# Kernel tuning notes

Measured on AMD Instinct MI355X. Metric: run time of the kernel, lower is better.

Reference implementation:

```python
import jax, jax.numpy as jnp
import numpy as np

N = 100000      # nodes
E = 1600000     # edges (avg degree 16)
D_IN, D_H, D_OUT = 128, 128, 64
EPS = 1e-5      # BatchNorm eps


def setup_inputs() -> dict:
    key = jax.random.key(0)
    ks = jax.random.split(key, 16)
    def w(k, i, o):
        return jax.random.normal(k, (i, o), jnp.float32) / np.float32(np.sqrt(i))
    inp = {
        "x": jax.random.normal(ks[0], (N, D_IN), jnp.float32),
        "edge_index": jax.random.randint(ks[1], (2, E), 0, N, dtype=jnp.int32),
        # layer 0 (SAGEConv: lin_l on aggregated neighbors w/ bias, lin_r on root w/o bias)
        "Wl0": w(ks[2], D_IN, D_H), "bl0": jax.random.normal(ks[3], (D_H,), jnp.float32) * 0.01,
        "Wr0": w(ks[4], D_IN, D_H),
        "g0": jnp.ones((D_H,), jnp.float32), "b0": jnp.zeros((D_H,), jnp.float32),
        "m0": jax.random.normal(ks[5], (D_H,), jnp.float32) * 0.1, "v0": jnp.ones((D_H,), jnp.float32),
        # layer 1
        "Wl1": w(ks[6], D_H, D_H), "bl1": jax.random.normal(ks[7], (D_H,), jnp.float32) * 0.01,
        "Wr1": w(ks[8], D_H, D_H),
        "g1": jnp.ones((D_H,), jnp.float32), "b1": jnp.zeros((D_H,), jnp.float32),
        "m1": jax.random.normal(ks[9], (D_H,), jnp.float32) * 0.1, "v1": jnp.ones((D_H,), jnp.float32),
        # layer 2 (output)
        "Wl2": w(ks[10], D_H, D_OUT), "bl2": jax.random.normal(ks[11], (D_OUT,), jnp.float32) * 0.01,
        "Wr2": w(ks[12], D_H, D_OUT),
    }
    return inp


def _sage_conv(x, src, dst, Wl, bl, Wr):
    # mean aggregation of neighbor (source) features at destination nodes
    deg = jax.ops.segment_sum(jnp.ones((src.shape[0],), x.dtype), dst, num_segments=N)
    agg = jax.ops.segment_sum(x[src], dst, num_segments=N)  # [N, d] irregular scatter-add
    agg = agg / jnp.maximum(deg, 1.0)[:, None]
    return agg @ Wl + bl + x @ Wr


def _bn(h, g, b, m, v):
    # BatchNorm1d in eval mode (running stats)
    return g * (h - m) * jax.lax.rsqrt(v + EPS) + b


def reference(x, edge_index,
              Wl0, bl0, Wr0, g0, b0, m0, v0,
              Wl1, bl1, Wr1, g1, b1, m1, v1,
              Wl2, bl2, Wr2):
    src, dst = edge_index[0], edge_index[1]
    h = jax.nn.relu(_bn(_sage_conv(x, src, dst, Wl0, bl0, Wr0), g0, b0, m0, v0))
    h = jax.nn.relu(_bn(_sage_conv(h, src, dst, Wl1, bl1, Wr1), g1, b1, m1, v1))
    h = _sage_conv(h, src, dst, Wl2, bl2, Wr2)
    return jax.nn.log_softmax(h, axis=-1)
```

## Files before the change

kernel.cpp:

```cpp
#include <hip/hip_runtime.h>

constexpr float EPS = 1e-5f;

#define NPB_LOG 9
#define NPB 512

typedef __attribute__((ext_vector_type(8))) __bf16 bf16x8;
typedef __attribute__((ext_vector_type(4))) float f32x4;
typedef __attribute__((ext_vector_type(2))) float f32x2;

__device__ __forceinline__ float blo(unsigned u) { return __uint_as_float(u << 16); }
__device__ __forceinline__ float bhi(unsigned u) { return __uint_as_float(u & 0xffff0000u); }
__device__ __forceinline__ unsigned bf1(float f) {
    unsigned u = __float_as_uint(f);
    return (u + 0x7fffu + ((u >> 16) & 1u)) >> 16;
}
__device__ __forceinline__ unsigned pack2(float a, float b) { return bf1(a) | (bf1(b) << 16); }

__device__ __forceinline__ f32x2 fp8lo(unsigned w) {
    return __builtin_amdgcn_cvt_pk_f32_fp8(w, false);
}
__device__ __forceinline__ f32x2 fp8hi(unsigned w) {
    return __builtin_amdgcn_cvt_pk_f32_fp8(w, true);
}


__global__ void bucket_hist_kernel(const int* __restrict__ dst, int* __restrict__ bcnt,
                                   int E, int B) {
    __shared__ int h[256];
    int t = threadIdx.x;
    h[t] = 0;
    __syncthreads();
    for (int e = blockIdx.x * blockDim.x + t; e < E; e += gridDim.x * blockDim.x)
        atomicAdd(&h[dst[e] >> NPB_LOG], 1);
    __syncthreads();
    if (t < B && h[t]) atomicAdd(&bcnt[t], h[t]);
}

__global__ void bucket_scan_kernel(const int* __restrict__ bcnt, int* __restrict__ bstart,
                                   int* __restrict__ cursorB, int B, int E) {
    __shared__ int tmp[256];
    int t = threadIdx.x;
    int v = (t < B) ? bcnt[t] : 0;
    tmp[t] = v;
    __syncthreads();
    for (int off = 1; off < 256; off <<= 1) {
        int x = tmp[t];
        if (t >= off) x += tmp[t - off];
        __syncthreads();
        tmp[t] = x;
        __syncthreads();
    }
    if (t < B) {
        int ex = tmp[t] - v;
        bstart[t] = ex;
        cursorB[t] = ex;
    }
    if (t == 0) bstart[B] = E;
}

__global__ __launch_bounds__(256) void partition_kernel(
    const int* __restrict__ src, const int* __restrict__ dst,
    int* __restrict__ cursorB, unsigned* __restrict__ ebuf, int E, int B) {
    __shared__ int hist[256];
    __shared__ int base[256];
    int t = threadIdx.x;
    hist[t] = 0;
    __syncthreads();
    int e0 = blockIdx.x * 4096;
    int e1 = min(e0 + 4096, E);
    for (int e = e0 + t; e < e1; e += 256)
        atomicAdd(&hist[dst[e] >> NPB_LOG], 1);
    __syncthreads();
    int h = hist[t];
    if (t < B && h) base[t] = atomicAdd(&cursorB[t], h);
    __syncthreads();
    hist[t] = 0;
    __syncthreads();
    for (int e = e0 + t; e < e1; e += 256) {
        int d = dst[e];
        int b = d >> NPB_LOG;
        int off = atomicAdd(&hist[b], 1);
        ebuf[base[b] + off] = ((unsigned)src[e] << NPB_LOG) | (unsigned)(d & (NPB - 1));
    }
}

__global__ __launch_bounds__(256) void build_csr_kernel(
    const unsigned* __restrict__ ebuf, const int* __restrict__ bstart,
    int* __restrict__ rowptr, float* __restrict__ degInv, int* __restrict__ csr,
    int N, int B) {
    __shared__ int cnt[NPB];
    __shared__ int cur[NPB];
    __shared__ int ps[256];
    int b = blockIdx.x;
    int t = threadIdx.x;
    int nbase = b << NPB_LOG;
    int nn = min(NPB, N - nbase);
    cnt[t] = 0;
    cnt[t + 256] = 0;
    __syncthreads();
    int ebeg = bstart[b], eend = bstart[b + 1];
    for (int e = ebeg + t; e < eend; e += 256)
        atomicAdd(&cnt[ebuf[e] & (NPB - 1)], 1);
    __syncthreads();
    int c0 = cnt[2 * t], c1 = cnt[2 * t + 1];
    int pair = c0 + c1;
    ps[t] = pair;
    __syncthreads();
    for (int off = 1; off < 256; off <<= 1) {
        int x = ps[t];
        if (t >= off) x += ps[t - off];
        __syncthreads();
        ps[t] = x;
        __syncthreads();
    }
    int exPair = ps[t] - pair;
    int g0 = ebeg + exPair;
    int g1 = g0 + c0;
    cur[2 * t] = g0;
    cur[2 * t + 1] = g1;
    if (2 * t < nn) {
        rowptr[nbase + 2 * t] = g0;
        degInv[nbase + 2 * t] = 1.0f / (float)max(c0, 1);
    }
    if (2 * t + 1 < nn) {
        rowptr[nbase + 2 * t + 1] = g1;
        degInv[nbase + 2 * t + 1] = 1.0f / (float)max(c1, 1);
    }
    if (b == B - 1 && t == 0) rowptr[N] = eend;
    __syncthreads();
    for (int e = ebeg + t; e < eend; e += 256) {
        unsigned p = ebuf[e];
        int pos = atomicAdd(&cur[p & (NPB - 1)], 1);
        csr[pos] = (int)(p >> NPB_LOG);
    }
}

__global__ void cvt_bf16_kernel(const float* __restrict__ in, unsigned short* __restrict__ out,
                                int n4) {
    int i = blockIdx.x * blockDim.x + threadIdx.x;
    if (i < n4) {
        float4 v = reinterpret_cast<const float4*>(in)[i];
        uint2 o;
        o.x = pack2(v.x, v.y);
        o.y = pack2(v.z, v.w);
        reinterpret_cast<uint2*>(out)[i] = o;
    }
}

__global__ void swizzleWcat_kernel(const float* __restrict__ Wl, const float* __restrict__ Wr,
                                   unsigned short* __restrict__ out, int K, int CL, int CR) {
    int C = CL + CR;
    int CT = C >> 4;
    int total = (K >> 5) * CT * 64;
    int id = blockIdx.x * blockDim.x + threadIdx.x;
    if (id >= total) return;
    int lane = id & 63;
    int ctkt = id >> 6;
    int ct = ctkt % CT;
    int kt = ctkt / CT;
    int col = ct * 16 + (lane & 15);
    int k0 = kt * 32 + (lane >> 4) * 8;
#pragma unroll
    for (int i = 0; i < 8; ++i) {
        int k = k0 + i;
        float w = (col < CL) ? Wl[(size_t)k * CL + col] : Wr[(size_t)k * CR + (col - CL)];
        out[(size_t)id * 8 + i] = (unsigned short)bf1(w);
    }
}

__global__ void bnprep_kernel(const float* __restrict__ g, const float* __restrict__ b,
                              const float* __restrict__ m, const float* __restrict__ v,
                              float* __restrict__ bnA, float* __restrict__ bnB, int D) {
    int c = blockIdx.x * blockDim.x + threadIdx.x;
    if (c < D) {
        float A = g[c] * rsqrtf(v[c] + EPS);
        bnA[c] = A;
        bnB[c] = b[c] - m[c] * A;
    }
}

template <int CHALF>
__global__ __launch_bounds__(256) void gemmT_kernel(
    const unsigned short* __restrict__ A, const unsigned short* __restrict__ Wsw,
    const float* __restrict__ bl,
    unsigned char* __restrict__ tL, unsigned short* __restrict__ tR, int n) {
    constexpr int CT = CHALF / 16;
    int tid = threadIdx.x;
    int lane = tid & 63;
    int wave = tid >> 6;
    int wr = wave >> 1, wc = wave & 1;
    int row0 = blockIdx.x * 64 + wr * 32;
    int rlo = lane & 15, kq = lane >> 4;

    f32x4 acc[2][CT];
#pragma unroll
    for (int nt = 0; nt < 2; ++nt)
#pragma unroll
        for (int c = 0; c < CT; ++c)
#pragma unroll
            for (int k = 0; k < 4; ++k) acc[nt][c][k] = 0.f;

    int r0 = row0 + rlo;
    int r1 = row0 + 16 + rlo;

    for (int kt = 0; kt < 4; ++kt) {
        int kb = kt * 32 + kq * 8;
        bf16x8 a0, a1;
#pragma unroll
        for (int i = 0; i < 8; ++i) { a0[i] = (__bf16)0.f; a1[i] = (__bf16)0.f; }
        if (r0 < n) a0 = *reinterpret_cast<const bf16x8*>(A + (size_t)r0 * 128 + kb);
        if (r1 < n) a1 = *reinterpret_cast<const bf16x8*>(A + (size_t)r1 * 128 + kb);
#pragma unroll
        for (int c = 0; c < CT; ++c) {
            int ct_g = wc * CT + c;
            bf16x8 w = *reinterpret_cast<const bf16x8*>(Wsw + ((size_t)(kt * 2 * CT + ct_g) * 64 + lane) * 8);
            acc[0][c] = __builtin_amdgcn_mfma_f32_16x16x32_bf16(w, a0, acc[0][c], 0, 0, 0);
            acc[1][c] = __builtin_amdgcn_mfma_f32_16x16x32_bf16(w, a1, acc[1][c], 0, 0, 0);
        }
    }

#pragma unroll
    for (int nt = 0; nt < 2; ++nt) {
        int r = row0 + nt * 16 + rlo;
        if (r >= n) continue;
#pragma unroll
        for (int c = 0; c < CT; ++c) {
            int colbase = c * 16 + kq * 4;
            if (wc == 0) {
                unsigned w = __builtin_amdgcn_cvt_pk_fp8_f32(acc[nt][c][0], acc[nt][c][1], 0, false);
                w = __builtin_amdgcn_cvt_pk_fp8_f32(acc[nt][c][2], acc[nt][c][3], w, true);
                *reinterpret_cast<unsigned*>(tL + (size_t)r * CHALF + colbase) = w;
            } else {
                float4 bv = *reinterpret_cast<const float4*>(bl + colbase);
                uint2 o;
                o.x = pack2(acc[nt][c][0] + bv.x, acc[nt][c][1] + bv.y);
                o.y = pack2(acc[nt][c][2] + bv.z, acc[nt][c][3] + bv.w);
                *reinterpret_cast<uint2*>(tR + (size_t)r * CHALF + colbase) = o;
            }
        }
    }
}

__global__ void aggbn_kernel(const unsigned char* __restrict__ tL,
                             const unsigned short* __restrict__ tR,
                             const float* __restrict__ bnA, const float* __restrict__ bnB,
                             const int* __restrict__ rowptr, const int* __restrict__ csr,
                             const float* __restrict__ degInv,
                             unsigned short* __restrict__ h, int n) {
    int idx = blockIdx.x * blockDim.x + threadIdx.x;
    int v = idx >> 4;
    int t = idx & 15;
    if (v >= n) return;
    int beg = rowptr[v], end = rowptr[v + 1];
    const uint2* T2 = reinterpret_cast<const uint2*>(tL);
    float s0 = 0.f, s1 = 0.f, s2 = 0.f, s3 = 0.f, s4 = 0.f, s5 = 0.f, s6 = 0.f, s7 = 0.f;
    int e = beg;
    for (; e + 4 <= end; e += 4) {
        uint2 w0 = T2[(size_t)csr[e + 0] * 16 + t];
        uint2 w1 = T2[(size_t)csr[e + 1] * 16 + t];
        uint2 w2 = T2[(size_t)csr[e + 2] * 16 + t];
        uint2 w3 = T2[(size_t)csr[e + 3] * 16 + t];
        f32x2 p;
        p = fp8lo(w0.x); s0 += p[0]; s1 += p[1];
        p = fp8hi(w0.x); s2 += p[0]; s3 += p[1];
        p = fp8lo(w0.y); s4 += p[0]; s5 += p[1];
        p = fp8hi(w0.y); s6 += p[0]; s7 += p[1];
        p = fp8lo(w1.x); s0 += p[0]; s1 += p[1];
        p = fp8hi(w1.x); s2 += p[0]; s3 += p[1];
        p = fp8lo(w1.y); s4 += p[0]; s5 += p[1];
        p = fp8hi(w1.y); s6 += p[0]; s7 += p[1];
        p = fp8lo(w2.x); s0 += p[0]; s1 += p[1];
        p = fp8hi(w2.x); s2 += p[0]; s3 += p[1];
        p = fp8lo(w2.y); s4 += p[0]; s5 += p[1];
        p = fp8hi(w2.y); s6 += p[0]; s7 += p[1];
        p = fp8lo(w3.x); s0 += p[0]; s1 += p[1];
        p = fp8hi(w3.x); s2 += p[0]; s3 += p[1];
        p = fp8lo(w3.y); s4 += p[0]; s5 += p[1];
        p = fp8hi(w3.y); s6 += p[0]; s7 += p[1];
    }
    for (; e < end; ++e) {
        uint2 w = T2[(size_t)csr[e] * 16 + t];
        f32x2 p;
        p = fp8lo(w.x); s0 += p[0]; s1 += p[1];
        p = fp8hi(w.x); s2 += p[0]; s3 += p[1];
        p = fp8lo(w.y); s4 += p[0]; s5 += p[1];
        p = fp8hi(w.y); s6 += p[0]; s7 += p[1];
    }
    float di = degInv[v];
    uint4 rw = reinterpret_cast<const uint4*>(tR)[(size_t)v * 16 + t];
    float4 A0 = reinterpret_cast<const float4*>(bnA + t * 8)[0];
    float4 A1 = reinterpret_cast<const float4*>(bnA + t * 8)[1];
    float4 B0 = reinterpret_cast<const float4*>(bnB + t * 8)[0];
    float4 B1 = reinterpret_cast<const float4*>(bnB + t * 8)[1];
    float h0 = fmaxf(A0.x * (s0 * di + blo(rw.x)) + B0.x, 0.f);
    float h1 = fmaxf(A0.y * (s1 * di + bhi(rw.x)) + B0.y, 0.f);
    float h2 = fmaxf(A0.z * (s2 * di + blo(rw.y)) + B0.z, 0.f);
    float h3 = fmaxf(A0.w * (s3 * di + bhi(rw.y)) + B0.w, 0.f);
    float h4 = fmaxf(A1.x * (s4 * di + blo(rw.z)) + B1.x, 0.f);
    float h5 = fmaxf(A1.y * (s5 * di + bhi(rw.z)) + B1.y, 0.f);
    float h6 = fmaxf(A1.z * (s6 * di + blo(rw.w)) + B1.z, 0.f);
    float h7 = fmaxf(A1.w * (s7 * di + bhi(rw.w)) + B1.w, 0.f);
    uint4 o;
    o.x = pack2(h0, h1);
    o.y = pack2(h2, h3);
    o.z = pack2(h4, h5);
    o.w = pack2(h6, h7);
    reinterpret_cast<uint4*>(h)[(size_t)v * 16 + t] = o;
}

__global__ void agg64_lsm_kernel(const unsigned char* __restrict__ tL2,
                                 const unsigned short* __restrict__ tR2,
                                 const int* __restrict__ rowptr, const int* __restrict__ csr,
                                 const float* __restrict__ degInv,
                                 float* __restrict__ out, int n) {
    int idx = blockIdx.x * blockDim.x + threadIdx.x;
    int v = idx >> 3;
    int t = idx & 7;
    if (v >= n) return;
    int beg = rowptr[v], end = rowptr[v + 1];
    const uint2* T2 = reinterpret_cast<const uint2*>(tL2);
    float s0 = 0.f, s1 = 0.f, s2 = 0.f, s3 = 0.f, s4 = 0.f, s5 = 0.f, s6 = 0.f, s7 = 0.f;
    int e = beg;
    for (; e + 4 <= end; e += 4) {
        uint2 w0 = T2[(size_t)csr[e + 0] * 8 + t];
        uint2 w1 = T2[(size_t)csr[e + 1] * 8 + t];
        uint2 w2 = T2[(size_t)csr[e + 2] * 8 + t];
        uint2 w3 = T2[(size_t)csr[e + 3] * 8 + t];
        f32x2 p;
        p = fp8lo(w0.x); s0 += p[0]; s1 += p[1];
        p = fp8hi(w0.x); s2 += p[0]; s3 += p[1];
        p = fp8lo(w0.y); s4 += p[0]; s5 += p[1];
        p = fp8hi(w0.y); s6 += p[0]; s7 += p[1];
        p = fp8lo(w1.x); s0 += p[0]; s1 += p[1];
        p = fp8hi(w1.x); s2 += p[0]; s3 += p[1];
        p = fp8lo(w1.y); s4 += p[0]; s5 += p[1];
        p = fp8hi(w1.y); s6 += p[0]; s7 += p[1];
        p = fp8lo(w2.x); s0 += p[0]; s1 += p[1];
        p = fp8hi(w2.x); s2 += p[0]; s3 += p[1];
        p = fp8lo(w2.y); s4 += p[0]; s5 += p[1];
        p = fp8hi(w2.y); s6 += p[0]; s7 += p[1];
        p = fp8lo(w3.x); s0 += p[0]; s1 += p[1];
        p = fp8hi(w3.x); s2 += p[0]; s3 += p[1];
        p = fp8lo(w3.y); s4 += p[0]; s5 += p[1];
        p = fp8hi(w3.y); s6 += p[0]; s7 += p[1];
    }
    for (; e < end; ++e) {
        uint2 w = T2[(size_t)csr[e] * 8 + t];
        f32x2 p;
        p = fp8lo(w.x); s0 += p[0]; s1 += p[1];
        p = fp8hi(w.x); s2 += p[0]; s3 += p[1];
        p = fp8lo(w.y); s4 += p[0]; s5 += p[1];
        p = fp8hi(w.y); s6 += p[0]; s7 += p[1];
    }
    float di = degInv[v];
    uint4 rw = reinterpret_cast<const uint4*>(tR2)[(size_t)v * 8 + t];
    float y0 = s0 * di + blo(rw.x);
    float y1 = s1 * di + bhi(rw.x);
    float y2 = s2 * di + blo(rw.y);
    float y3 = s3 * di + bhi(rw.y);
    float y4 = s4 * di + blo(rw.z);
    float y5 = s5 * di + bhi(rw.z);
    float y6 = s6 * di + blo(rw.w);
    float y7 = s7 * di + bhi(rw.w);

    float mx = fmaxf(fmaxf(fmaxf(y0, y1), fmaxf(y2, y3)),
                     fmaxf(fmaxf(y4, y5), fmaxf(y6, y7)));
#pragma unroll
    for (int o = 1; o < 8; o <<= 1) mx = fmaxf(mx, __shfl_xor(mx, o));
    float s = __expf(y0 - mx) + __expf(y1 - mx) + __expf(y2 - mx) + __expf(y3 - mx)
            + __expf(y4 - mx) + __expf(y5 - mx) + __expf(y6 - mx) + __expf(y7 - mx);
#pragma unroll
    for (int o = 1; o < 8; o <<= 1) s += __shfl_xor(s, o);
    float lse = mx + __logf(s);

    float4 oA, oB;
    oA.x = y0 - lse; oA.y = y1 - lse; oA.z = y2 - lse; oA.w = y3 - lse;
    oB.x = y4 - lse; oB.y = y5 - lse; oB.z = y6 - lse; oB.w = y7 - lse;
    float4* O4 = reinterpret_cast<float4*>(out + (size_t)v * 64 + t * 8);
    O4[0] = oA;
    O4[1] = oB;
}


extern "C" void kernel_launch(void* const* d_in, const int* in_sizes, int n_in,
                              void* d_out, int out_size, void* d_ws, size_t ws_size,
                              hipStream_t stream) {
    const float* x   = (const float*)d_in[0];
    const int*   ei  = (const int*)d_in[1];
    const float* Wl0 = (const float*)d_in[2];
    const float* bl0 = (const float*)d_in[3];
    const float* Wr0 = (const float*)d_in[4];
    const float* g0  = (const float*)d_in[5];
    const float* b0  = (const float*)d_in[6];
    const float* m0  = (const float*)d_in[7];
    const float* v0  = (const float*)d_in[8];
    const float* Wl1 = (const float*)d_in[9];
    const float* bl1 = (const float*)d_in[10];
    const float* Wr1 = (const float*)d_in[11];
    const float* g1  = (const float*)d_in[12];
    const float* b1  = (const float*)d_in[13];
    const float* m1  = (const float*)d_in[14];
    const float* v1  = (const float*)d_in[15];
    const float* Wl2 = (const float*)d_in[16];
    const float* bl2 = (const float*)d_in[17];
    const float* Wr2 = (const float*)d_in[18];
    float* out = (float*)d_out;

    const int N = in_sizes[0] / 128;
    const int E = in_sizes[1] / 2;
    const int B = (N + NPB - 1) >> NPB_LOG;
    const int* src = ei;
    const int* dst = ei + E;

    char* ws = (char*)d_ws;
    size_t off = 0;
    auto alloc = [&](size_t bytes) -> void* {
        void* p = ws + off;
        off += (bytes + 255) & ~(size_t)255;
        return p;
    };
    int*   bcnt    = (int*)alloc(256 * 4);
    int*   bstart  = (int*)alloc(257 * 4);
    int*   cursorB = (int*)alloc(256 * 4);
    int*   rowptr  = (int*)alloc((size_t)(N + 1) * 4);
    float* degInv  = (float*)alloc((size_t)N * 4);
    int*   csr     = (int*)alloc((size_t)E * 4);
    unsigned* ebuf = (unsigned*)alloc((size_t)E * 4);
    unsigned short* x16 = (unsigned short*)alloc((size_t)N * 128 * 2);
    unsigned short* hA  = (unsigned short*)alloc((size_t)N * 128 * 2);
    unsigned short* hB  = (unsigned short*)alloc((size_t)N * 128 * 2);
    unsigned char*  tL  = (unsigned char*)alloc((size_t)N * 128);
    unsigned short* tR  = (unsigned short*)alloc((size_t)N * 128 * 2);
    unsigned short* Wsw0 = (unsigned short*)alloc(4 * 16 * 64 * 8 * 2);
    unsigned short* Wsw1 = (unsigned short*)alloc(4 * 16 * 64 * 8 * 2);
    unsigned short* Wsw2 = (unsigned short*)alloc(4 * 8 * 64 * 8 * 2);
    float* bnA0 = (float*)alloc(128 * 4);
    float* bnB0 = (float*)alloc(128 * 4);
    float* bnA1 = (float*)alloc(128 * 4);
    float* bnB1 = (float*)alloc(128 * 4);
    unsigned char*  tL2 = tL;
    unsigned short* tR2 = tR;

    hipMemsetAsync(bcnt, 0, 256 * 4, stream);

    bucket_hist_kernel<<<512, 256, 0, stream>>>(dst, bcnt, E, B);
    bucket_scan_kernel<<<1, 256, 0, stream>>>(bcnt, bstart, cursorB, B, E);
    partition_kernel<<<(E + 4095) / 4096, 256, 0, stream>>>(src, dst, cursorB, ebuf, E, B);
    build_csr_kernel<<<B, 256, 0, stream>>>(ebuf, bstart, rowptr, degInv, csr, N, B);

    int n4 = N * 32;
    cvt_bf16_kernel<<<(n4 + 255) / 256, 256, 0, stream>>>(x, x16, n4);
    swizzleWcat_kernel<<<16, 256, 0, stream>>>(Wl0, Wr0, Wsw0, 128, 128, 128);
    swizzleWcat_kernel<<<16, 256, 0, stream>>>(Wl1, Wr1, Wsw1, 128, 128, 128);
    swizzleWcat_kernel<<<8, 256, 0, stream>>>(Wl2, Wr2, Wsw2, 128, 64, 64);
    bnprep_kernel<<<1, 128, 0, stream>>>(g0, b0, m0, v0, bnA0, bnB0, 128);
    bnprep_kernel<<<1, 128, 0, stream>>>(g1, b1, m1, v1, bnA1, bnB1, 128);

    int gemmGrid = (N + 63) / 64;
    int aggGrid = (int)(((size_t)N * 16 + 255) / 256);
    int lsmGrid = (int)(((size_t)N * 8 + 255) / 256);

    gemmT_kernel<128><<<gemmGrid, 256, 0, stream>>>(x16, Wsw0, bl0, tL, tR, N);
    aggbn_kernel<<<aggGrid, 256, 0, stream>>>(tL, tR, bnA0, bnB0, rowptr, csr, degInv, hA, N);
    gemmT_kernel<128><<<gemmGrid, 256, 0, stream>>>(hA, Wsw1, bl1, tL, tR, N);
    aggbn_kernel<<<aggGrid, 256, 0, stream>>>(tL, tR, bnA1, bnB1, rowptr, csr, degInv, hB, N);
    gemmT_kernel<64><<<gemmGrid, 256, 0, stream>>>(hB, Wsw2, bl2, tL2, tR2, N);
    agg64_lsm_kernel<<<lsmGrid, 256, 0, stream>>>(tL2, tR2, rowptr, csr, degInv, out, N);
}
```

Baseline: 285.8 us.

## Vectorize edge preprocessing, fuse fp32 conversion into GEMM, merge prep kernels, unroll gathers

Edge bucketing, partitioning and CSR construction now read indices as uint4 vectors, with scalar head and tail loops. The separate fp32-to-bf16 conversion kernel is removed: the first GEMM reads x in fp32 and converts in registers, which drops one full pass over the node features. The weight swizzle and BatchNorm prep launches are merged into one kernel, and the neighbor gather loops are unrolled from 4 to 8 to keep more loads in flight. The risks are higher register pressure in the aggregation kernels and the first GEMM reading twice as many A bytes.

```diff
diff --git a/kernel.cpp b/kernel.cpp
--- a/kernel.cpp
+++ b/kernel.cpp
@@ -31,8 +31,17 @@
     int t = threadIdx.x;
     h[t] = 0;
     __syncthreads();
-    for (int e = blockIdx.x * blockDim.x + t; e < E; e += gridDim.x * blockDim.x)
-        atomicAdd(&h[dst[e] >> NPB_LOG], 1);
+    int E4 = E >> 2;
+    const uint4* d4 = reinterpret_cast<const uint4*>(dst);
+    for (int i = blockIdx.x * blockDim.x + t; i < E4; i += gridDim.x * blockDim.x) {
+        uint4 d = d4[i];
+        atomicAdd(&h[d.x >> NPB_LOG], 1);
+        atomicAdd(&h[d.y >> NPB_LOG], 1);
+        atomicAdd(&h[d.z >> NPB_LOG], 1);
+        atomicAdd(&h[d.w >> NPB_LOG], 1);
+    }
+    if (blockIdx.x == 0 && t < (E & 3))
+        atomicAdd(&h[dst[E4 * 4 + t] >> NPB_LOG], 1);
     __syncthreads();
     if (t < B && h[t]) atomicAdd(&bcnt[t], h[t]);
 }
@@ -69,7 +78,18 @@
     __syncthreads();
     int e0 = blockIdx.x * 4096;
     int e1 = min(e0 + 4096, E);
-    for (int e = e0 + t; e < e1; e += 256)
+    const uint4* d4 = reinterpret_cast<const uint4*>(dst);
+    const uint4* s4 = reinterpret_cast<const uint4*>(src);
+    int n4 = (e1 - e0) >> 2;
+    int i0 = e0 >> 2;
+    for (int i = t; i < n4; i += 256) {
+        uint4 d = d4[i0 + i];
+        atomicAdd(&hist[d.x >> NPB_LOG], 1);
+        atomicAdd(&hist[d.y >> NPB_LOG], 1);
+        atomicAdd(&hist[d.z >> NPB_LOG], 1);
+        atomicAdd(&hist[d.w >> NPB_LOG], 1);
+    }
+    for (int e = e0 + n4 * 4 + t; e < e1; e += 256)
         atomicAdd(&hist[dst[e] >> NPB_LOG], 1);
     __syncthreads();
     int h = hist[t];
@@ -77,7 +97,20 @@
     __syncthreads();
     hist[t] = 0;
     __syncthreads();
-    for (int e = e0 + t; e < e1; e += 256) {
+    for (int i = t; i < n4; i += 256) {
+        uint4 d = d4[i0 + i];
+        uint4 s = s4[i0 + i];
+        int b0i = d.x >> NPB_LOG, b1i = d.y >> NPB_LOG, b2i = d.z >> NPB_LOG, b3i = d.w >> NPB_LOG;
+        int o0 = atomicAdd(&hist[b0i], 1);
+        ebuf[base[b0i] + o0] = (s.x << NPB_LOG) | (d.x & (NPB - 1));
+        int o1 = atomicAdd(&hist[b1i], 1);
+        ebuf[base[b1i] + o1] = (s.y << NPB_LOG) | (d.y & (NPB - 1));
+        int o2 = atomicAdd(&hist[b2i], 1);
+        ebuf[base[b2i] + o2] = (s.z << NPB_LOG) | (d.z & (NPB - 1));
+        int o3 = atomicAdd(&hist[b3i], 1);
+        ebuf[base[b3i] + o3] = (s.w << NPB_LOG) | (d.w & (NPB - 1));
+    }
+    for (int e = e0 + n4 * 4 + t; e < e1; e += 256) {
         int d = dst[e];
         int b = d >> NPB_LOG;
         int off = atomicAdd(&hist[b], 1);
@@ -100,7 +133,19 @@
     cnt[t + 256] = 0;
     __syncthreads();
     int ebeg = bstart[b], eend = bstart[b + 1];
-    for (int e = ebeg + t; e < eend; e += 256)
+    int eh = min((4 - (ebeg & 3)) & 3, eend - ebeg) + ebeg;
+    for (int e = ebeg + t; e < eh; e += 256)
+        atomicAdd(&cnt[ebuf[e] & (NPB - 1)], 1);
+    int n4 = (eend - eh) >> 2;
+    const uint4* p4 = reinterpret_cast<const uint4*>(ebuf + eh);
+    for (int i = t; i < n4; i += 256) {
+        uint4 p = p4[i];
+        atomicAdd(&cnt[p.x & (NPB - 1)], 1);
+        atomicAdd(&cnt[p.y & (NPB - 1)], 1);
+        atomicAdd(&cnt[p.z & (NPB - 1)], 1);
+        atomicAdd(&cnt[p.w & (NPB - 1)], 1);
+    }
+    for (int e = eh + n4 * 4 + t; e < eend; e += 256)
         atomicAdd(&cnt[ebuf[e] & (NPB - 1)], 1);
     __syncthreads();
     int c0 = cnt[2 * t], c1 = cnt[2 * t + 1];
@@ -129,32 +174,30 @@
     }
     if (b == B - 1 && t == 0) rowptr[N] = eend;
     __syncthreads();
-    for (int e = ebeg + t; e < eend; e += 256) {
+    for (int e = ebeg + t; e < eh; e += 256) {
         unsigned p = ebuf[e];
         int pos = atomicAdd(&cur[p & (NPB - 1)], 1);
         csr[pos] = (int)(p >> NPB_LOG);
     }
-}
-
-__global__ void cvt_bf16_kernel(const float* __restrict__ in, unsigned short* __restrict__ out,
-                                int n4) {
-    int i = blockIdx.x * blockDim.x + threadIdx.x;
-    if (i < n4) {
-        float4 v = reinterpret_cast<const float4*>(in)[i];
-        uint2 o;
-        o.x = pack2(v.x, v.y);
-        o.y = pack2(v.z, v.w);
-        reinterpret_cast<uint2*>(out)[i] = o;
-    }
-}
-
-__global__ void swizzleWcat_kernel(const float* __restrict__ Wl, const float* __restrict__ Wr,
-                                   unsigned short* __restrict__ out, int K, int CL, int CR) {
+    for (int i = t; i < n4; i += 256) {
+        uint4 p = p4[i];
+        int pos;
+        pos = atomicAdd(&cur[p.x & (NPB - 1)], 1); csr[pos] = (int)(p.x >> NPB_LOG);
+        pos = atomicAdd(&cur[p.y & (NPB - 1)], 1); csr[pos] = (int)(p.y >> NPB_LOG);
+        pos = atomicAdd(&cur[p.z & (NPB - 1)], 1); csr[pos] = (int)(p.z >> NPB_LOG);
+        pos = atomicAdd(&cur[p.w & (NPB - 1)], 1); csr[pos] = (int)(p.w >> NPB_LOG);
+    }
+    for (int e = eh + n4 * 4 + t; e < eend; e += 256) {
+        unsigned p = ebuf[e];
+        int pos = atomicAdd(&cur[p & (NPB - 1)], 1);
+        csr[pos] = (int)(p >> NPB_LOG);
+    }
+}
+
+__device__ __forceinline__ void swz_one(const float* __restrict__ Wl, const float* __restrict__ Wr,
+                                        unsigned short* __restrict__ out, int CL, int CR, int id) {
     int C = CL + CR;
     int CT = C >> 4;
-    int total = (K >> 5) * CT * 64;
-    int id = blockIdx.x * blockDim.x + threadIdx.x;
-    if (id >= total) return;
     int lane = id & 63;
     int ctkt = id >> 6;
     int ct = ctkt % CT;
@@ -169,20 +212,42 @@
     }
 }
 
-__global__ void bnprep_kernel(const float* __restrict__ g, const float* __restrict__ b,
-                              const float* __restrict__ m, const float* __restrict__ v,
-                              float* __restrict__ bnA, float* __restrict__ bnB, int D) {
-    int c = blockIdx.x * blockDim.x + threadIdx.x;
-    if (c < D) {
-        float A = g[c] * rsqrtf(v[c] + EPS);
-        bnA[c] = A;
-        bnB[c] = b[c] - m[c] * A;
-    }
-}
-
-template <int CHALF>
+__global__ void prep_kernel(const float* __restrict__ Wl0, const float* __restrict__ Wr0,
+                            const float* __restrict__ Wl1, const float* __restrict__ Wr1,
+                            const float* __restrict__ Wl2, const float* __restrict__ Wr2,
+                            const float* __restrict__ g0, const float* __restrict__ b0,
+                            const float* __restrict__ m0, const float* __restrict__ v0,
+                            const float* __restrict__ g1, const float* __restrict__ b1,
+                            const float* __restrict__ m1, const float* __restrict__ v1,
+                            unsigned short* __restrict__ Wsw0, unsigned short* __restrict__ Wsw1,
+                            unsigned short* __restrict__ Wsw2,
+                            float* __restrict__ bnA0, float* __restrict__ bnB0,
+                            float* __restrict__ bnA1, float* __restrict__ bnB1) {
+    int bid = blockIdx.x;
+    int t = threadIdx.x;
+    if (bid < 16) {
+        swz_one(Wl0, Wr0, Wsw0, 128, 128, bid * 256 + t);
+    } else if (bid < 32) {
+        swz_one(Wl1, Wr1, Wsw1, 128, 128, (bid - 16) * 256 + t);
+    } else if (bid < 40) {
+        swz_one(Wl2, Wr2, Wsw2, 64, 64, (bid - 32) * 256 + t);
+    } else {
+        if (t < 128) {
+            float A = g0[t] * rsqrtf(v0[t] + EPS);
+            bnA0[t] = A;
+            bnB0[t] = b0[t] - m0[t] * A;
+        } else {
+            int c = t - 128;
+            float A = g1[c] * rsqrtf(v1[c] + EPS);
+            bnA1[c] = A;
+            bnB1[c] = b1[c] - m1[c] * A;
+        }
+    }
+}
+
+template <int CHALF, bool AF32>
 __global__ __launch_bounds__(256) void gemmT_kernel(
-    const unsigned short* __restrict__ A, const unsigned short* __restrict__ Wsw,
+    const void* __restrict__ Av, const unsigned short* __restrict__ Wsw,
     const float* __restrict__ bl,
     unsigned char* __restrict__ tL, unsigned short* __restrict__ tR, int n) {
     constexpr int CT = CHALF / 16;
@@ -209,8 +274,25 @@
         bf16x8 a0, a1;
 #pragma unroll
         for (int i = 0; i < 8; ++i) { a0[i] = (__bf16)0.f; a1[i] = (__bf16)0.f; }
-        if (r0 < n) a0 = *reinterpret_cast<const bf16x8*>(A + (size_t)r0 * 128 + kb);
-        if (r1 < n) a1 = *reinterpret_cast<const bf16x8*>(A + (size_t)r1 * 128 + kb);
+        if (AF32) {
+            const float* Af = (const float*)Av;
+            if (r0 < n) {
+                float4 f0 = *reinterpret_cast<const float4*>(Af + (size_t)r0 * 128 + kb);
+                float4 f1 = *reinterpret_cast<const float4*>(Af + (size_t)r0 * 128 + kb + 4);
+                a0[0] = (__bf16)f0.x; a0[1] = (__bf16)f0.y; a0[2] = (__bf16)f0.z; a0[3] = (__bf16)f0.w;
+                a0[4] = (__bf16)f1.x; a0[5] = (__bf16)f1.y; a0[6] = (__bf16)f1.z; a0[7] = (__bf16)f1.w;
+            }
+            if (r1 < n) {
+                float4 f0 = *reinterpret_cast<const float4*>(Af + (size_t)r1 * 128 + kb);
+                float4 f1 = *reinterpret_cast<const float4*>(Af + (size_t)r1 * 128 + kb + 4);
+                a1[0] = (__bf16)f0.x; a1[1] = (__bf16)f0.y; a1[2] = (__bf16)f0.z; a1[3] = (__bf16)f0.w;
+                a1[4] = (__bf16)f1.x; a1[5] = (__bf16)f1.y; a1[6] = (__bf16)f1.z; a1[7] = (__bf16)f1.w;
+            }
+        } else {
+            const unsigned short* A = (const unsigned short*)Av;
+            if (r0 < n) a0 = *reinterpret_cast<const bf16x8*>(A + (size_t)r0 * 128 + kb);
+            if (r1 < n) a1 = *reinterpret_cast<const bf16x8*>(A + (size_t)r1 * 128 + kb);
+        }
 #pragma unroll
         for (int c = 0; c < CT; ++c) {
             int ct_g = wc * CT + c;
@@ -256,11 +338,15 @@
     const uint2* T2 = reinterpret_cast<const uint2*>(tL);
     float s0 = 0.f, s1 = 0.f, s2 = 0.f, s3 = 0.f, s4 = 0.f, s5 = 0.f, s6 = 0.f, s7 = 0.f;
     int e = beg;
-    for (; e + 4 <= end; e += 4) {
+    for (; e + 8 <= end; e += 8) {
         uint2 w0 = T2[(size_t)csr[e + 0] * 16 + t];
         uint2 w1 = T2[(size_t)csr[e + 1] * 16 + t];
         uint2 w2 = T2[(size_t)csr[e + 2] * 16 + t];
         uint2 w3 = T2[(size_t)csr[e + 3] * 16 + t];
+        uint2 w4 = T2[(size_t)csr[e + 4] * 16 + t];
+        uint2 w5 = T2[(size_t)csr[e + 5] * 16 + t];
+        uint2 w6 = T2[(size_t)csr[e + 6] * 16 + t];
+        uint2 w7 = T2[(size_t)csr[e + 7] * 16 + t];
         f32x2 p;
         p = fp8lo(w0.x); s0 += p[0]; s1 += p[1];
         p = fp8hi(w0.x); s2 += p[0]; s3 += p[1];
@@ -278,6 +364,22 @@
         p = fp8hi(w3.x); s2 += p[0]; s3 += p[1];
         p = fp8lo(w3.y); s4 += p[0]; s5 += p[1];
         p = fp8hi(w3.y); s6 += p[0]; s7 += p[1];
+        p = fp8lo(w4.x); s0 += p[0]; s1 += p[1];
+        p = fp8hi(w4.x); s2 += p[0]; s3 += p[1];
+        p = fp8lo(w4.y); s4 += p[0]; s5 += p[1];
+        p = fp8hi(w4.y); s6 += p[0]; s7 += p[1];
+        p = fp8lo(w5.x); s0 += p[0]; s1 += p[1];
+        p = fp8hi(w5.x); s2 += p[0]; s3 += p[1];
+        p = fp8lo(w5.y); s4 += p[0]; s5 += p[1];
+        p = fp8hi(w5.y); s6 += p[0]; s7 += p[1];
+        p = fp8lo(w6.x); s0 += p[0]; s1 += p[1];
+        p = fp8hi(w6.x); s2 += p[0]; s3 += p[1];
+        p = fp8lo(w6.y); s4 += p[0]; s5 += p[1];
+        p = fp8hi(w6.y); s6 += p[0]; s7 += p[1];
+        p = fp8lo(w7.x); s0 += p[0]; s1 += p[1];
+        p = fp8hi(w7.x); s2 += p[0]; s3 += p[1];
+        p = fp8lo(w7.y); s4 += p[0]; s5 += p[1];
+        p = fp8hi(w7.y); s6 += p[0]; s7 += p[1];
     }
     for (; e < end; ++e) {
         uint2 w = T2[(size_t)csr[e] * 16 + t];
@@ -322,11 +424,15 @@
     const uint2* T2 = reinterpret_cast<const uint2*>(tL2);
     float s0 = 0.f, s1 = 0.f, s2 = 0.f, s3 = 0.f, s4 = 0.f, s5 = 0.f, s6 = 0.f, s7 = 0.f;
     int e = beg;
-    for (; e + 4 <= end; e += 4) {
+    for (; e + 8 <= end; e += 8) {
         uint2 w0 = T2[(size_t)csr[e + 0] * 8 + t];
         uint2 w1 = T2[(size_t)csr[e + 1] * 8 + t];
         uint2 w2 = T2[(size_t)csr[e + 2] * 8 + t];
         uint2 w3 = T2[(size_t)csr[e + 3] * 8 + t];
+        uint2 w4 = T2[(size_t)csr[e + 4] * 8 + t];
+        uint2 w5 = T2[(size_t)csr[e + 5] * 8 + t];
+        uint2 w6 = T2[(size_t)csr[e + 6] * 8 + t];
+        uint2 w7 = T2[(size_t)csr[e + 7] * 8 + t];
         f32x2 p;
         p = fp8lo(w0.x); s0 += p[0]; s1 += p[1];
         p = fp8hi(w0.x); s2 += p[0]; s3 += p[1];
@@ -344,6 +450,22 @@
         p = fp8hi(w3.x); s2 += p[0]; s3 += p[1];
         p = fp8lo(w3.y); s4 += p[0]; s5 += p[1];
         p = fp8hi(w3.y); s6 += p[0]; s7 += p[1];
+        p = fp8lo(w4.x); s0 += p[0]; s1 += p[1];
+        p = fp8hi(w4.x); s2 += p[0]; s3 += p[1];
+        p = fp8lo(w4.y); s4 += p[0]; s5 += p[1];
+        p = fp8hi(w4.y); s6 += p[0]; s7 += p[1];
+        p = fp8lo(w5.x); s0 += p[0]; s1 += p[1];
+        p = fp8hi(w5.x); s2 += p[0]; s3 += p[1];
+        p = fp8lo(w5.y); s4 += p[0]; s5 += p[1];
+        p = fp8hi(w5.y); s6 += p[0]; s7 += p[1];
+        p = fp8lo(w6.x); s0 += p[0]; s1 += p[1];
+        p = fp8hi(w6.x); s2 += p[0]; s3 += p[1];
+        p = fp8lo(w6.y); s4 += p[0]; s5 += p[1];
+        p = fp8hi(w6.y); s6 += p[0]; s7 += p[1];
+        p = fp8lo(w7.x); s0 += p[0]; s1 += p[1];
+        p = fp8hi(w7.x); s2 += p[0]; s3 += p[1];
+        p = fp8lo(w7.y); s4 += p[0]; s5 += p[1];
+        p = fp8hi(w7.y); s6 += p[0]; s7 += p[1];
     }
     for (; e < end; ++e) {
         uint2 w = T2[(size_t)csr[e] * 8 + t];
@@ -427,7 +549,6 @@
     float* degInv  = (float*)alloc((size_t)N * 4);
     int*   csr     = (int*)alloc((size_t)E * 4);
     unsigned* ebuf = (unsigned*)alloc((size_t)E * 4);
-    unsigned short* x16 = (unsigned short*)alloc((size_t)N * 128 * 2);
     unsigned short* hA  = (unsigned short*)alloc((size_t)N * 128 * 2);
     unsigned short* hB  = (unsigned short*)alloc((size_t)N * 128 * 2);
     unsigned char*  tL  = (unsigned char*)alloc((size_t)N * 128);
@@ -448,23 +569,18 @@
     bucket_scan_kernel<<<1, 256, 0, stream>>>(bcnt, bstart, cursorB, B, E);
     partition_kernel<<<(E + 4095) / 4096, 256, 0, stream>>>(src, dst, cursorB, ebuf, E, B);
     build_csr_kernel<<<B, 256, 0, stream>>>(ebuf, bstart, rowptr, degInv, csr, N, B);
-
-    int n4 = N * 32;
-    cvt_bf16_kernel<<<(n4 + 255) / 256, 256, 0, stream>>>(x, x16, n4);
-    swizzleWcat_kernel<<<16, 256, 0, stream>>>(Wl0, Wr0, Wsw0, 128, 128, 128);
-    swizzleWcat_kernel<<<16, 256, 0, stream>>>(Wl1, Wr1, Wsw1, 128, 128, 128);
-    swizzleWcat_kernel<<<8, 256, 0, stream>>>(Wl2, Wr2, Wsw2, 128, 64, 64);
-    bnprep_kernel<<<1, 128, 0, stream>>>(g0, b0, m0, v0, bnA0, bnB0, 128);
-    bnprep_kernel<<<1, 128, 0, stream>>>(g1, b1, m1, v1, bnA1, bnB1, 128);
+    prep_kernel<<<41, 256, 0, stream>>>(Wl0, Wr0, Wl1, Wr1, Wl2, Wr2,
+                                        g0, b0, m0, v0, g1, b1, m1, v1,
+                                        Wsw0, Wsw1, Wsw2, bnA0, bnB0, bnA1, bnB1);
 
     int gemmGrid = (N + 63) / 64;
     int aggGrid = (int)(((size_t)N * 16 + 255) / 256);
     int lsmGrid = (int)(((size_t)N * 8 + 255) / 256);
 
-    gemmT_kernel<128><<<gemmGrid, 256, 0, stream>>>(x16, Wsw0, bl0, tL, tR, N);
+    gemmT_kernel<128, true><<<gemmGrid, 256, 0, stream>>>(x, Wsw0, bl0, tL, tR, N);
     aggbn_kernel<<<aggGrid, 256, 0, stream>>>(tL, tR, bnA0, bnB0, rowptr, csr, degInv, hA, N);
-    gemmT_kernel<128><<<gemmGrid, 256, 0, stream>>>(hA, Wsw1, bl1, tL, tR, N);
+    gemmT_kernel<128, false><<<gemmGrid, 256, 0, stream>>>(hA, Wsw1, bl1, tL, tR, N);
     aggbn_kernel<<<aggGrid, 256, 0, stream>>>(tL, tR, bnA1, bnB1, rowptr, csr, degInv, hB, N);
-    gemmT_kernel<64><<<gemmGrid, 256, 0, stream>>>(hB, Wsw2, bl2, tL2, tR2, N);
+    gemmT_kernel<64, false><<<gemmGrid, 256, 0, stream>>>(hB, Wsw2, bl2, tL2, tR2, N);
     agg64_lsm_kernel<<<lsmGrid, 256, 0, stream>>>(tL2, tR2, rowptr, csr, degInv, out, N);
 }
```

Measured after the change: 260.2 us. 9.0% less time.
